# Optimization experiments

Hardware: AMD Instinct MI355X
Metric: run time of the kernel (lower is better)

The kernel has to match this reference:

```python
import jax, jax.numpy as jnp
import numpy as np

CONSTRAINT_WEIGHT = 0.05
MAX_ATOMIC_NUM = 119  # lookup table size; unknown types default to valence 4


def _valence_table(dtype):
    t = np.full((MAX_ATOMIC_NUM,), 4.0, dtype=np.float32)
    for z, v in {1: 1, 6: 4, 7: 3, 8: 2, 9: 1, 15: 5, 16: 6, 17: 7}.items():
        t[z] = v
    return jnp.asarray(t, dtype=dtype)


def setup_inputs() -> dict:
    key = jax.random.key(0)
    k1, k2, k3 = jax.random.split(key, 3)
    N, E, D = 100000, 3200000, 256
    h = jax.random.normal(k1, (N, D), dtype=jnp.float32)
    edge_index = jax.random.randint(k2, (2, E), 0, N, dtype=jnp.int64)
    atom_types = jax.random.randint(k3, (N,), 0, 18, dtype=jnp.int64)
    return {"h": h, "edge_index": edge_index, "atom_types": atom_types}


def reference(h, edge_index, atom_types):
    N = h.shape[0]
    row = edge_index[0]
    # bond count per atom: scatter-add of ones over edge source indices
    bond_counts = jnp.zeros((N,), dtype=h.dtype).at[row].add(jnp.asarray(1.0, h.dtype))
    # vectorized valence-table gather (replaces per-atom Python loop)
    max_val = _valence_table(h.dtype)[jnp.clip(atom_types, 0, MAX_ATOMIC_NUM - 1)]
    violation = jnp.maximum(bond_counts - max_val, 0.0)  # [N]
    constraint_loss = jnp.mean(violation) * jnp.asarray(CONSTRAINT_WEIGHT, h.dtype)
    # scale violating atoms' features by (1 - 0.1 * violation)
    penalty = jnp.where(violation > 0, 1.0 - violation * 0.1, 1.0).astype(h.dtype)
    h_new = h * penalty[:, None]
    return h_new, constraint_loss
```

## Files before the change

kernel.cpp:

```cpp
#include <hip/hip_runtime.h>


typedef float floatx4 __attribute__((ext_vector_type(4)));
typedef int   intx4   __attribute__((ext_vector_type(4)));

__device__ __forceinline__ float max_valence(int z) {
    switch (z) {
        case 1:  return 1.0f;
        case 6:  return 4.0f;
        case 7:  return 3.0f;
        case 8:  return 2.0f;
        case 9:  return 1.0f;
        case 15: return 5.0f;
        case 16: return 6.0f;
        case 17: return 7.0f;
        default: return 4.0f;
    }
}

#define VC_WR 12512

__global__ void vc_count_lds(const int* __restrict__ row, int E, int chunk,
                             unsigned int* __restrict__ slices,
                             int RA, int NR, int WR, int W2,
                             float* __restrict__ accum) {
    __shared__ unsigned int lds[VC_WR];
    const int b = blockIdx.x;
    if (b == 0 && threadIdx.x == 0) *accum = 0.0f;
    const int start = b * chunk;
    const int end   = min(start + chunk, E);
    const int nq    = max(end - start, 0) >> 2;
    const intx4* q  = reinterpret_cast<const intx4*>(row + start);
    unsigned int* slice = slices + (size_t)b * W2;

    for (int r = 0; r < NR; ++r) {
        const int lo = r * RA;
        for (int i = threadIdx.x; i < WR; i += blockDim.x) lds[i] = 0;
        __syncthreads();
        for (int i = threadIdx.x; i < nq; i += blockDim.x) {
            intx4 e = __builtin_nontemporal_load(&q[i]);
            int a;
            a = e.x - lo; if ((unsigned)a < (unsigned)RA)
                atomicAdd(&lds[a >> 3], 1u << ((a & 7) << 2));
            a = e.y - lo; if ((unsigned)a < (unsigned)RA)
                atomicAdd(&lds[a >> 3], 1u << ((a & 7) << 2));
            a = e.z - lo; if ((unsigned)a < (unsigned)RA)
                atomicAdd(&lds[a >> 3], 1u << ((a & 7) << 2));
            a = e.w - lo; if ((unsigned)a < (unsigned)RA)
                atomicAdd(&lds[a >> 3], 1u << ((a & 7) << 2));
        }
        for (int i = start + (nq << 2) + threadIdx.x; i < end; i += blockDim.x) {
            int a = row[i] - lo;
            if ((unsigned)a < (unsigned)RA)
                atomicAdd(&lds[a >> 3], 1u << ((a & 7) << 2));
        }
        __syncthreads();
        for (int i = threadIdx.x; i < WR; i += blockDim.x)
            slice[r * WR + i] = lds[i];
        if (r + 1 < NR) __syncthreads();
    }
}

__global__ void vc_merge(const unsigned int* __restrict__ slices,
                         int C, int W2,
                         const int* __restrict__ types, int N,
                         float* __restrict__ penalty,
                         float* __restrict__ accum) {
    const int a = blockIdx.x * blockDim.x + threadIdx.x;
    float vsum = 0.0f;
    if (a < N) {
        const unsigned int* p = slices + (a >> 3);
        const int sh = (a & 7) << 2;
        unsigned int cnt = 0;
        int c = 0;
        #pragma unroll 1
        for (; c + 8 <= C; c += 8) {
            unsigned int x0 = p[(size_t)(c + 0) * W2];
            unsigned int x1 = p[(size_t)(c + 1) * W2];
            unsigned int x2 = p[(size_t)(c + 2) * W2];
            unsigned int x3 = p[(size_t)(c + 3) * W2];
            unsigned int x4 = p[(size_t)(c + 4) * W2];
            unsigned int x5 = p[(size_t)(c + 5) * W2];
            unsigned int x6 = p[(size_t)(c + 6) * W2];
            unsigned int x7 = p[(size_t)(c + 7) * W2];
            cnt += (x0 >> sh) & 0xFu;
            cnt += (x1 >> sh) & 0xFu;
            cnt += (x2 >> sh) & 0xFu;
            cnt += (x3 >> sh) & 0xFu;
            cnt += (x4 >> sh) & 0xFu;
            cnt += (x5 >> sh) & 0xFu;
            cnt += (x6 >> sh) & 0xFu;
            cnt += (x7 >> sh) & 0xFu;
        }
        for (; c < C; ++c) cnt += (p[(size_t)c * W2] >> sh) & 0xFu;
        float v = fmaxf((float)cnt - max_valence(types[a]), 0.0f);
        vsum = v;
        penalty[a] = (v > 0.0f) ? (1.0f - v * 0.1f) : 1.0f;
    }
    #pragma unroll
    for (int off = 32; off > 0; off >>= 1) vsum += __shfl_down(vsum, off, 64);
    __shared__ float sh4[4];
    int lane = threadIdx.x & 63;
    int wv   = threadIdx.x >> 6;
    if (lane == 0) sh4[wv] = vsum;
    __syncthreads();
    if (threadIdx.x == 0) atomicAdd(accum, sh4[0] + sh4[1] + sh4[2] + sh4[3]);
}

__global__ void vc_scale(const floatx4* __restrict__ h,
                         const float* __restrict__ penalty,
                         floatx4* __restrict__ out,
                         int nquads, int qpr, int qshift,
                         const float* __restrict__ accum,
                         float* __restrict__ out_loss, float lscale) {
    if (blockIdx.x == 0 && threadIdx.x == 0) *out_loss = (*accum) * lscale;
    int t = blockIdx.x * (blockDim.x * 4) + threadIdx.x;
    #pragma unroll
    for (int k = 0; k < 4; ++k, t += blockDim.x) {
        if (t < nquads) {
            int rowi = (qshift >= 0) ? (t >> qshift) : (t / qpr);
            float p = penalty[rowi];
            floatx4 x = __builtin_nontemporal_load(&h[t]);
            x *= p;
            __builtin_nontemporal_store(x, &out[t]);
        }
    }
}

extern "C" void kernel_launch(void* const* d_in, const int* in_sizes, int n_in,
                              void* d_out, int out_size, void* d_ws, size_t ws_size,
                              hipStream_t stream) {
    const float* h          = (const float*)d_in[0];
    const int*   edge_index = (const int*)d_in[1];
    const int*   atom_types = (const int*)d_in[2];

    const int N = in_sizes[2];
    const int D = in_sizes[0] / N;
    const int E = in_sizes[1] / 2;

    const int NR = (N + VC_WR * 8 - 1) / (VC_WR * 8);
    const int RA = (((N + NR - 1) / NR) + 7) & ~7;
    const int WR = RA / 8;
    const int W2 = NR * WR;

    int C = 256;
    {
        long long avail = (long long)ws_size - 64 - (long long)N * 4 - 16;
        long long cmax  = avail / ((long long)W2 * 4);
        if (cmax < C) C = (int)cmax;
        if (C < 1) C = 1;
    }

    const size_t slices_bytes = (((size_t)C * W2 * 4) + 15) & ~(size_t)15;
    float*        accum   = (float*)d_ws;
    unsigned int* slices  = (unsigned int*)((char*)d_ws + 64);
    float*        penalty = (float*)((char*)d_ws + 64 + slices_bytes);

    float* out_h    = (float*)d_out;
    float* out_loss = out_h + (size_t)N * D;

    {
        int chunk = ((E + C - 1) / C + 3) & ~3;
        vc_count_lds<<<C, 1024, 0, stream>>>(edge_index, E, chunk, slices,
                                             RA, NR, WR, W2, accum);
    }

    {
        int blocks = (N + 255) / 256;
        vc_merge<<<blocks, 256, 0, stream>>>(slices, C, W2, atom_types, N,
                                             penalty, accum);
    }

    {
        int nquads = (N * D) / 4;
        int qpr = D / 4;
        int qshift = (qpr > 0 && (qpr & (qpr - 1)) == 0) ? __builtin_ctz(qpr) : -1;
        int blocks = (nquads + 1023) / 1024;
        vc_scale<<<blocks, 256, 0, stream>>>(
            (const floatx4*)h, penalty, (floatx4*)out_h, nquads, qpr, qshift,
            accum, out_loss, 0.05f / (float)N);
    }
}
```

Measured before the change: 212.2 us.

## Fuse merge and scale kernels with per-block penalties and ticket-based loss finalize

Merges the slice-merge and row-scaling kernels into one kernel. Each block handles 64 atoms, and its four waves split the slice-count reduction four ways, combining partial counts through LDS atomics. Penalties stay in LDS, so there is no global penalty buffer and one launch is removed. The loss is finalized by the last block to take a ticket counter, which adds a threadfence and atomic per block.

```diff
diff --git a/kernel.cpp b/kernel.cpp
--- a/kernel.cpp
+++ b/kernel.cpp
@@ -19,14 +19,16 @@
 }
 
 #define VC_WR 12512
+#define VC_AB 64
 
 __global__ void vc_count_lds(const int* __restrict__ row, int E, int chunk,
                              unsigned int* __restrict__ slices,
                              int RA, int NR, int WR, int W2,
-                             float* __restrict__ accum) {
+                             float* __restrict__ accum,
+                             unsigned int* __restrict__ ticket) {
     __shared__ unsigned int lds[VC_WR];
     const int b = blockIdx.x;
-    if (b == 0 && threadIdx.x == 0) *accum = 0.0f;
+    if (b == 0 && threadIdx.x == 0) { *accum = 0.0f; *ticket = 0u; }
     const int start = b * chunk;
     const int end   = min(start + chunk, E);
     const int nq    = max(end - start, 0) >> 2;
@@ -61,20 +63,32 @@
     }
 }
 
-__global__ void vc_merge(const unsigned int* __restrict__ slices,
-                         int C, int W2,
-                         const int* __restrict__ types, int N,
-                         float* __restrict__ penalty,
-                         float* __restrict__ accum) {
-    const int a = blockIdx.x * blockDim.x + threadIdx.x;
-    float vsum = 0.0f;
+__global__ __launch_bounds__(256) void vc_fused(
+        const unsigned int* __restrict__ slices, int C, int W2,
+        const int* __restrict__ types, int N,
+        const floatx4* __restrict__ h, floatx4* __restrict__ out,
+        int qpr, int qshift,
+        float* __restrict__ accum, unsigned int* __restrict__ ticket,
+        float* __restrict__ out_loss, float lscale) {
+    __shared__ unsigned int cntLds[VC_AB];
+    __shared__ float penLds[VC_AB];
+    const int a0 = blockIdx.x * VC_AB;
+    const int wv = threadIdx.x >> 6;
+    const int al = threadIdx.x & 63;
+    const int a  = a0 + al;
+
+    if (threadIdx.x < VC_AB) cntLds[threadIdx.x] = 0u;
+    __syncthreads();
+
+    unsigned int cnt = 0u;
     if (a < N) {
         const unsigned int* p = slices + (a >> 3);
         const int sh = (a & 7) << 2;
-        unsigned int cnt = 0;
-        int c = 0;
+        const int CQ = (C + 3) >> 2;
+        int c = wv * CQ;
+        const int ce = min(c + CQ, C);
         #pragma unroll 1
-        for (; c + 8 <= C; c += 8) {
+        for (; c + 8 <= ce; c += 8) {
             unsigned int x0 = p[(size_t)(c + 0) * W2];
             unsigned int x1 = p[(size_t)(c + 1) * W2];
             unsigned int x2 = p[(size_t)(c + 2) * W2];
@@ -92,38 +106,46 @@
             cnt += (x6 >> sh) & 0xFu;
             cnt += (x7 >> sh) & 0xFu;
         }
-        for (; c < C; ++c) cnt += (p[(size_t)c * W2] >> sh) & 0xFu;
-        float v = fmaxf((float)cnt - max_valence(types[a]), 0.0f);
-        vsum = v;
-        penalty[a] = (v > 0.0f) ? (1.0f - v * 0.1f) : 1.0f;
+        for (; c < ce; ++c) cnt += (p[(size_t)c * W2] >> sh) & 0xFu;
+        if (cnt) atomicAdd(&cntLds[al], cnt);
     }
-    #pragma unroll
-    for (int off = 32; off > 0; off >>= 1) vsum += __shfl_down(vsum, off, 64);
-    __shared__ float sh4[4];
-    int lane = threadIdx.x & 63;
-    int wv   = threadIdx.x >> 6;
-    if (lane == 0) sh4[wv] = vsum;
     __syncthreads();
-    if (threadIdx.x == 0) atomicAdd(accum, sh4[0] + sh4[1] + sh4[2] + sh4[3]);
-}
 
-__global__ void vc_scale(const floatx4* __restrict__ h,
-                         const float* __restrict__ penalty,
-                         floatx4* __restrict__ out,
-                         int nquads, int qpr, int qshift,
-                         const float* __restrict__ accum,
-                         float* __restrict__ out_loss, float lscale) {
-    if (blockIdx.x == 0 && threadIdx.x == 0) *out_loss = (*accum) * lscale;
-    int t = blockIdx.x * (blockDim.x * 4) + threadIdx.x;
-    #pragma unroll
-    for (int k = 0; k < 4; ++k, t += blockDim.x) {
-        if (t < nquads) {
-            int rowi = (qshift >= 0) ? (t >> qshift) : (t / qpr);
-            float p = penalty[rowi];
-            floatx4 x = __builtin_nontemporal_load(&h[t]);
-            x *= p;
-            __builtin_nontemporal_store(x, &out[t]);
+    float vsum = 0.0f;
+    if (threadIdx.x < VC_AB) {
+        const int aa = a0 + threadIdx.x;
+        float pen = 1.0f;
+        if (aa < N) {
+            float v = fmaxf((float)cntLds[threadIdx.x] - max_valence(types[aa]), 0.0f);
+            vsum = v;
+            pen = (v > 0.0f) ? (1.0f - v * 0.1f) : 1.0f;
         }
+        penLds[threadIdx.x] = pen;
+    }
+    if (wv == 0) {
+        #pragma unroll
+        for (int off = 32; off > 0; off >>= 1) vsum += __shfl_down(vsum, off, 64);
+        if (threadIdx.x == 0 && vsum != 0.0f) atomicAdd(accum, vsum);
+        if (threadIdx.x == 0) {
+            __threadfence();
+            unsigned int t = atomicAdd(ticket, 1u);
+            if (t == gridDim.x - 1u) {
+                float tot = atomicAdd(accum, 0.0f);
+                *out_loss = tot * lscale;
+            }
+        }
+    }
+    __syncthreads();
+
+    const int rows   = min(VC_AB, N - a0);
+    const int nq_blk = rows * qpr;
+    const floatx4* hq = h   + (size_t)a0 * qpr;
+    floatx4*       oq = out + (size_t)a0 * qpr;
+    for (int i = threadIdx.x; i < nq_blk; i += 256) {
+        int r = (qshift >= 0) ? (i >> qshift) : (i / qpr);
+        floatx4 x = __builtin_nontemporal_load(&hq[i]);
+        x *= penLds[r];
+        __builtin_nontemporal_store(x, &oq[i]);
     }
 }
 
@@ -145,16 +167,15 @@
 
     int C = 256;
     {
-        long long avail = (long long)ws_size - 64 - (long long)N * 4 - 16;
+        long long avail = (long long)ws_size - 64 - 16;
         long long cmax  = avail / ((long long)W2 * 4);
         if (cmax < C) C = (int)cmax;
         if (C < 1) C = 1;
     }
 
-    const size_t slices_bytes = (((size_t)C * W2 * 4) + 15) & ~(size_t)15;
-    float*        accum   = (float*)d_ws;
-    unsigned int* slices  = (unsigned int*)((char*)d_ws + 64);
-    float*        penalty = (float*)((char*)d_ws + 64 + slices_bytes);
+    float*        accum  = (float*)d_ws;
+    unsigned int* ticket = (unsigned int*)((char*)d_ws + 4);
+    unsigned int* slices = (unsigned int*)((char*)d_ws + 64);
 
     float* out_h    = (float*)d_out;
     float* out_loss = out_h + (size_t)N * D;
@@ -162,22 +183,16 @@
     {
         int chunk = ((E + C - 1) / C + 3) & ~3;
         vc_count_lds<<<C, 1024, 0, stream>>>(edge_index, E, chunk, slices,
-                                             RA, NR, WR, W2, accum);
+                                             RA, NR, WR, W2, accum, ticket);
     }
 
     {
-        int blocks = (N + 255) / 256;
-        vc_merge<<<blocks, 256, 0, stream>>>(slices, C, W2, atom_types, N,
-                                             penalty, accum);
-    }
-
-    {
-        int nquads = (N * D) / 4;
         int qpr = D / 4;
         int qshift = (qpr > 0 && (qpr & (qpr - 1)) == 0) ? __builtin_ctz(qpr) : -1;
-        int blocks = (nquads + 1023) / 1024;
-        vc_scale<<<blocks, 256, 0, stream>>>(
-            (const floatx4*)h, penalty, (floatx4*)out_h, nquads, qpr, qshift,
-            accum, out_loss, 0.05f / (float)N);
+        int blocks = (N + VC_AB - 1) / VC_AB;
+        vc_fused<<<blocks, 256, 0, stream>>>(slices, C, W2, atom_types, N,
+                                             (const floatx4*)h, (floatx4*)out_h,
+                                             qpr, qshift, accum, ticket,
+                                             out_loss, 0.05f / (float)N);
     }
 }
```

New measurement: 272.2 us. +28.3%, slower.
